# Kernel tuning notes

Hardware: AMD Instinct MI355X
Metric: run time of the kernel (lower is better)

The kernel has to match this reference:

```python
import jax, jax.numpy as jnp
import numpy as np

B, L, C = 4, 4096, 64

def setup_inputs() -> dict:
    key = jax.random.key(0)
    ks = jax.random.split(key, 7)
    s = 1.0 / np.sqrt(C)
    return {
        "x": jax.random.normal(ks[0], (B, L, C), dtype=jnp.float32),
        "Wq": jax.random.normal(ks[1], (C, C), dtype=jnp.float32) * s,
        "bq": jnp.zeros((C,), dtype=jnp.float32),
        "Wk": jax.random.normal(ks[2], (C, C), dtype=jnp.float32) * s,
        "bk": jnp.zeros((C,), dtype=jnp.float32),
        "Wv": jax.random.normal(ks[3], (C, C), dtype=jnp.float32) * s,
        "bv": jnp.zeros((C,), dtype=jnp.float32),
    }

def reference(x, Wq, bq, Wk, bk, Wv, bv):
    # Conv1D kernel_size=1 == pointwise linear over channels
    Q = jnp.einsum('blc,cf->blf', x, Wq) + bq  # [B, L, F]
    K = jnp.einsum('blc,cf->blf', x, Wk) + bk
    V = jnp.einsum('blc,cf->blf', x, Wv) + bv
    F = Wq.shape[1]
    scores = jnp.einsum('bqf,bkf->bqk', Q, K) / jnp.sqrt(jnp.float32(F))  # [B, Lq, Lk]
    # NOTE: original uses tf.keras.layers.Softmax(axis=1) -> normalize over QUERY axis
    attn = jax.nn.softmax(scores, axis=1)
    out = jnp.einsum('bqk,bkf->bqf', attn, V)
    return out + x
```

## Files before the change

kernel.cpp:

```cpp
#include <hip/hip_runtime.h>
#include <math.h>


#define BB 4
#define LL 4096
#define CC 64
#define C2 0.18033688011112042f

typedef __attribute__((ext_vector_type(8)))  short bf16x8;
typedef __attribute__((ext_vector_type(4)))  float f32x4;
typedef __attribute__((ext_vector_type(16))) float f32x16;
typedef __attribute__((ext_vector_type(4)))  unsigned int u32x4;

#define MFMA16(a, b, c) __builtin_amdgcn_mfma_f32_16x16x32_bf16(a, b, c, 0, 0, 0)
#define MFMA32(a, b, c) __builtin_amdgcn_mfma_f32_32x32x16_bf16(a, b, c, 0, 0, 0)
#define EXP2(x) __builtin_amdgcn_exp2f(x)

#define GLDS(gp, lp) __builtin_amdgcn_global_load_lds( \
    (const __attribute__((address_space(1))) unsigned int*)(gp), \
    (__attribute__((address_space(3))) unsigned int*)(lp), 16, 0, 0)
#define WAITVM0() asm volatile("s_waitcnt vmcnt(0)" ::: "memory")
#define WAITVM4() asm volatile("s_waitcnt vmcnt(4)" ::: "memory")
#define WAITVM8() asm volatile("s_waitcnt vmcnt(8)" ::: "memory")
#define LGKM0()   asm volatile("s_waitcnt lgkmcnt(0)" ::: "memory")
#define SBAR() __builtin_amdgcn_sched_barrier(0)

static __device__ __forceinline__ bf16x8 asbf(u32x4 v) {
    union { u32x4 a; bf16x8 b; } u; u.a = v; return u.b;
}
static __device__ __forceinline__ unsigned short f2bf(float f) {
    union { float f; unsigned u; } v; v.f = f;
    unsigned r = v.u + 0x7FFFu + ((v.u >> 16) & 1u);
    return (unsigned short)(r >> 16);
}
static __device__ __forceinline__ float bf2f(unsigned short h) {
    union { unsigned u; float f; } v; v.u = ((unsigned)h) << 16; return v.f;
}
static __device__ __forceinline__ bf16x8 pack8(float4 a, float4 b) {
    bf16x8 r;
    r[0] = (short)f2bf(a.x); r[1] = (short)f2bf(a.y);
    r[2] = (short)f2bf(a.z); r[3] = (short)f2bf(a.w);
    r[4] = (short)f2bf(b.x); r[5] = (short)f2bf(b.y);
    r[6] = (short)f2bf(b.z); r[7] = (short)f2bf(b.w);
    return r;
}
static __device__ __forceinline__ unsigned cvtpk(float lo, float hi) {
    unsigned r;
    asm("v_cvt_pk_bf16_f32 %0, %1, %2" : "=v"(r) : "v"(lo), "v"(hi));
    return r;
}


__global__ __launch_bounds__(512) void k_qkv(
    const float* __restrict__ x,
    const float* __restrict__ Wq, const float* __restrict__ bq,
    const float* __restrict__ Wk, const float* __restrict__ bk,
    const float* __restrict__ Wv, const float* __restrict__ bv,
    unsigned short* __restrict__ Qb, unsigned short* __restrict__ Kb,
    unsigned short* __restrict__ Vt)
{
    __shared__ float Wl[64 * 64];
    __shared__ unsigned short ldsV[64 * 72];
    __shared__ unsigned short ldsF[4096];
    const int bid = blockIdx.x;
    const int mat = bid % 3;
    const int r0 = (bid / 3) * 64;
    const int tid = threadIdx.x, w = tid >> 6, lane = tid & 63;
    const int c = lane & 15, g = lane >> 4;
    const int rw = (w >> 1) * 16;
    const int c0 = (w & 1) * 32;

    const float* W  = (mat == 0) ? Wq : (mat == 1) ? Wk : Wv;
    const float* bs = (mat == 0) ? bq : (mat == 1) ? bk : bv;

    {
        const float4* wsrc = (const float4*)W;
        float4* wdst = (float4*)Wl;
        wdst[tid] = wsrc[tid];
        wdst[tid + 512] = wsrc[tid + 512];
    }

    const float* xr = x + (size_t)(r0 + rw + c) * CC;
    const bf16x8 ax0 = pack8(((const float4*)xr)[2 * g], ((const float4*)xr)[2 * g + 1]);
    const bf16x8 ax1 = pack8(((const float4*)xr)[8 + 2 * g], ((const float4*)xr)[8 + 2 * g + 1]);
    __syncthreads();

    f32x4 acc0 = {0.f, 0.f, 0.f, 0.f}, acc1 = {0.f, 0.f, 0.f, 0.f};
    {
        const int col = c0 + c;
        bf16x8 b0, b1;
        #pragma unroll
        for (int j = 0; j < 8; ++j) {
            b0[j] = (short)f2bf(Wl[(8 * g + j) * 64 + col]);
            b1[j] = (short)f2bf(Wl[(32 + 8 * g + j) * 64 + col]);
        }
        acc0 = MFMA16(ax0, b0, acc0); acc0 = MFMA16(ax1, b1, acc0);
    }
    {
        const int col = c0 + 16 + c;
        bf16x8 b0, b1;
        #pragma unroll
        for (int j = 0; j < 8; ++j) {
            b0[j] = (short)f2bf(Wl[(8 * g + j) * 64 + col]);
            b1[j] = (short)f2bf(Wl[(32 + 8 * g + j) * 64 + col]);
        }
        acc1 = MFMA16(ax0, b0, acc1); acc1 = MFMA16(ax1, b1, acc1);
    }
    const float bias0 = bs[c0 + c], bias1 = bs[c0 + 16 + c];

    if (mat < 2) {
        #pragma unroll
        for (int r = 0; r < 4; ++r) {
            const int row = rw + 4 * g + r;
            const int tl = row >> 5, lr = row & 31;
            const int col0 = c0 + c;
            ldsF[tl * 2048 + (col0 >> 4) * 512 + (((col0 >> 3) & 1) * 32 + lr) * 8 + (col0 & 7)]
                = f2bf(acc0[r] + bias0);
            const int col1 = c0 + 16 + c;
            ldsF[tl * 2048 + (col1 >> 4) * 512 + (((col1 >> 3) & 1) * 32 + lr) * 8 + (col1 & 7)]
                = f2bf(acc1[r] + bias1);
        }
        __syncthreads();
        unsigned short* dst = (mat == 0) ? Qb : Kb;
        *(uint4*)(dst + ((size_t)(r0 >> 5)) * 2048 + tid * 8) =
            *(const uint4*)(ldsF + tid * 8);
    } else {
        #pragma unroll
        for (int r = 0; r < 4; ++r) {
            const int rowin = rw + 4 * g + r;
            ldsV[(c0 + c) * 72 + rowin]      = f2bf(acc0[r] + bias0);
            ldsV[(c0 + 16 + c) * 72 + rowin] = f2bf(acc1[r] + bias1);
        }
        __syncthreads();
        const int b = r0 >> 12, ktb = (r0 & 4095) >> 5;
        const int f = tid >> 3, ch = tid & 7;
        const size_t dtile = (size_t)(b * 128 + ktb + (ch >> 2));
        const size_t didx = dtile * 2048
            + (size_t)(((f >> 5) * 2 + ((ch >> 1) & 1)) * 512
                       + ((ch & 1) * 32 + (f & 31)) * 8);
        *(uint4*)(Vt + didx) = *(const uint4*)(ldsV + f * 72 + ch * 8);
    }
}

__global__ __launch_bounds__(512, 2) void k_stats(
    const unsigned short* __restrict__ Qb, const unsigned short* __restrict__ Kb,
    unsigned short* __restrict__ Vt)
{
    const int nb = ((blockIdx.x & 7) << 5) | (blockIdx.x >> 3);
    const int b = nb >> 6, kt = nb & 63;
    const int tid = threadIdx.x, w = tid >> 6, lane = tid & 63;
    const int l31 = lane & 31, hi = lane >> 5;
    const int w_u = __builtin_amdgcn_readfirstlane(w);

    __shared__ unsigned short qsm[8][2][2048];
    __shared__ float pl[8][64];
    __shared__ float rls[64];

    const char* Kt = (const char*)Kb + ((size_t)(b * 128 + kt * 2)) * 4096 + lane * 16;
    const bf16x8 akA0 = *(const bf16x8*)(Kt);
    const bf16x8 akA1 = *(const bf16x8*)(Kt + 1024);
    const bf16x8 akA2 = *(const bf16x8*)(Kt + 2048);
    const bf16x8 akA3 = *(const bf16x8*)(Kt + 3072);
    const bf16x8 akB0 = *(const bf16x8*)(Kt + 4096);
    const bf16x8 akB1 = *(const bf16x8*)(Kt + 5120);
    const bf16x8 akB2 = *(const bf16x8*)(Kt + 6144);
    const bf16x8 akB3 = *(const bf16x8*)(Kt + 7168);

    const char* const gQ = (const char*)Qb + ((size_t)(b * 128 + w * 16)) * 4096 + lane * 16;

    #define QISS(s_, buf_) do { \
        const char* _g = gQ + (size_t)(s_) * 4096; \
        char* _l = (char*)&qsm[w_u][buf_][0]; \
        GLDS(_g, _l);              GLDS(_g + 1024, _l + 1024); \
        GLDS(_g + 2048, _l + 2048); GLDS(_g + 3072, _l + 3072); \
    } while (0)

    QISS(0, 0); QISS(1, 1);

    f32x16 laccA = {}, laccB = {};
    #pragma unroll 2
    for (int s = 0; s < 16; ++s) {
        const int buf = s & 1;
        if (s < 15) { WAITVM4(); } else { WAITVM0(); }
        SBAR();
        const char* qp = (const char*)&qsm[w_u][buf][0] + lane * 16;
        const bf16x8 q0 = *(const bf16x8*)(qp);
        const bf16x8 q1 = *(const bf16x8*)(qp + 1024);
        const bf16x8 q2 = *(const bf16x8*)(qp + 2048);
        const bf16x8 q3 = *(const bf16x8*)(qp + 3072);
        LGKM0(); SBAR();
        if (s < 14) QISS(s + 2, buf);
        f32x16 TA = {}, TB = {};
        TA = MFMA32(akA0, q0, TA); TA = MFMA32(akA1, q1, TA);
        TA = MFMA32(akA2, q2, TA); TA = MFMA32(akA3, q3, TA);
        TB = MFMA32(akB0, q0, TB); TB = MFMA32(akB1, q1, TB);
        TB = MFMA32(akB2, q2, TB); TB = MFMA32(akB3, q3, TB);
        #pragma unroll
        for (int r = 0; r < 16; ++r) {
            laccA[r] += EXP2(TA[r] * C2);
            laccB[r] += EXP2(TB[r] * C2);
        }
    }
    #undef QISS

    #pragma unroll
    for (int r = 0; r < 16; ++r) {
        float va = laccA[r], vb = laccB[r];
        va += __shfl_xor(va, 1);  vb += __shfl_xor(vb, 1);
        va += __shfl_xor(va, 2);  vb += __shfl_xor(vb, 2);
        va += __shfl_xor(va, 4);  vb += __shfl_xor(vb, 4);
        va += __shfl_xor(va, 8);  vb += __shfl_xor(vb, 8);
        va += __shfl_xor(va, 16); vb += __shfl_xor(vb, 16);
        laccA[r] = va; laccB[r] = vb;
    }
    if (l31 == 0) {
        #pragma unroll
        for (int r = 0; r < 16; ++r) {
            const int kr = (r & 3) + 8 * (r >> 2) + 4 * hi;
            pl[w][kr]      = laccA[r];
            pl[w][32 + kr] = laccB[r];
        }
    }
    __syncthreads();
    if (tid < 64) {
        float L = 0.f;
        #pragma unroll
        for (int ww = 0; ww < 8; ++ww) L += pl[ww][tid];
        rls[tid] = 1.0f / L;
    }
    __syncthreads();

    #pragma unroll
    for (int i = 0; i < 2; ++i) {
        unsigned short* base = Vt + ((size_t)(b * 128 + kt * 2 + i)) * 2048;
        const int frag = tid >> 7, lane16 = (tid & 127) >> 1, j0 = (tid & 1) * 4;
        const int kin = (frag & 1) * 16 + (lane16 >> 5) * 8 + j0;
        ushort4 v = *(const ushort4*)(base + tid * 4);
        v.x = f2bf(bf2f(v.x) * rls[i * 32 + kin + 0]);
        v.y = f2bf(bf2f(v.y) * rls[i * 32 + kin + 1]);
        v.z = f2bf(bf2f(v.z) * rls[i * 32 + kin + 2]);
        v.w = f2bf(bf2f(v.w) * rls[i * 32 + kin + 3]);
        *(ushort4*)(base + tid * 4) = v;
    }
}

__global__ __launch_bounds__(512, 2) void k_out(
    const float* __restrict__ x,
    const unsigned short* __restrict__ Qb, const unsigned short* __restrict__ Kb,
    const unsigned short* __restrict__ Vt,
    float* __restrict__ out)
{
    const int nb = ((blockIdx.x & 7) << 5) | (blockIdx.x >> 3);
    const int b = nb >> 6, qt = nb & 63;
    const int q0 = qt * 64;
    const int tid = threadIdx.x, w = tid >> 6, lane = tid & 63;
    const int l31 = lane & 31, hi = lane >> 5;
    const int w_u = __builtin_amdgcn_readfirstlane(w);

    __shared__ unsigned short ksm[8][2][2048];
    __shared__ unsigned short vsm[8][2][2048];

    const char* Qt0 = (const char*)Qb + ((size_t)(b * 128 + qt * 2)) * 4096 + lane * 16;
    const bf16x8 qA0 = *(const bf16x8*)(Qt0);
    const bf16x8 qA1 = *(const bf16x8*)(Qt0 + 1024);
    const bf16x8 qA2 = *(const bf16x8*)(Qt0 + 2048);
    const bf16x8 qA3 = *(const bf16x8*)(Qt0 + 3072);
    const bf16x8 qB0 = *(const bf16x8*)(Qt0 + 4096);
    const bf16x8 qB1 = *(const bf16x8*)(Qt0 + 5120);
    const bf16x8 qB2 = *(const bf16x8*)(Qt0 + 6144);
    const bf16x8 qB3 = *(const bf16x8*)(Qt0 + 7168);

    const char* const gK = (const char*)Kb + ((size_t)(b * 128 + w * 16)) * 4096 + lane * 16;
    const char* const gV = (const char*)Vt + ((size_t)(b * 128 + w * 16)) * 4096 + lane * 16;

    #define ISS(s_, buf_) do { \
        const char* _gk = gK + (size_t)(s_) * 4096; \
        const char* _gv = gV + (size_t)(s_) * 4096; \
        char* _lk = (char*)&ksm[w_u][buf_][0]; \
        char* _lv = (char*)&vsm[w_u][buf_][0]; \
        GLDS(_gk, _lk);              GLDS(_gk + 1024, _lk + 1024); \
        GLDS(_gk + 2048, _lk + 2048); GLDS(_gk + 3072, _lk + 3072); \
        GLDS(_gv, _lv);              GLDS(_gv + 1024, _lv + 1024); \
        GLDS(_gv + 2048, _lv + 2048); GLDS(_gv + 3072, _lv + 3072); \
    } while (0)

    ISS(0, 0); ISS(1, 1);

    f32x16 oA0 = {}, oA1 = {}, oB0 = {}, oB1 = {};

    #pragma unroll 2
    for (int s = 0; s < 16; ++s) {
        const int buf = s & 1;
        if (s < 15) { WAITVM8(); } else { WAITVM0(); }
        SBAR();
        const char* kp = (const char*)&ksm[w_u][buf][0] + lane * 16;
        const char* vp = (const char*)&vsm[w_u][buf][0] + lane * 16;
        const bf16x8 a0  = *(const bf16x8*)(kp);
        const bf16x8 a1  = *(const bf16x8*)(kp + 1024);
        const bf16x8 a2  = *(const bf16x8*)(kp + 2048);
        const bf16x8 a3  = *(const bf16x8*)(kp + 3072);
        const bf16x8 v00 = *(const bf16x8*)(vp);
        const bf16x8 v01 = *(const bf16x8*)(vp + 1024);
        const bf16x8 v10 = *(const bf16x8*)(vp + 2048);
        const bf16x8 v11 = *(const bf16x8*)(vp + 3072);
        LGKM0(); SBAR();
        if (s < 14) ISS(s + 2, buf);
        f32x16 TA = {}, TB = {};
        TA = MFMA32(a0, qA0, TA); TA = MFMA32(a1, qA1, TA);
        TA = MFMA32(a2, qA2, TA); TA = MFMA32(a3, qA3, TA);
        TB = MFMA32(a0, qB0, TB); TB = MFMA32(a1, qB1, TB);
        TB = MFMA32(a2, qB2, TB); TB = MFMA32(a3, qB3, TB);
        unsigned a0u = cvtpk(EXP2(TA[0] * C2),  EXP2(TA[1] * C2));
        unsigned a1u = cvtpk(EXP2(TA[2] * C2),  EXP2(TA[3] * C2));
        unsigned a2u = cvtpk(EXP2(TA[4] * C2),  EXP2(TA[5] * C2));
        unsigned a3u = cvtpk(EXP2(TA[6] * C2),  EXP2(TA[7] * C2));
        unsigned a4u = cvtpk(EXP2(TA[8] * C2),  EXP2(TA[9] * C2));
        unsigned a5u = cvtpk(EXP2(TA[10] * C2), EXP2(TA[11] * C2));
        unsigned a6u = cvtpk(EXP2(TA[12] * C2), EXP2(TA[13] * C2));
        unsigned a7u = cvtpk(EXP2(TA[14] * C2), EXP2(TA[15] * C2));
        unsigned b0u = cvtpk(EXP2(TB[0] * C2),  EXP2(TB[1] * C2));
        unsigned b1u = cvtpk(EXP2(TB[2] * C2),  EXP2(TB[3] * C2));
        unsigned b2u = cvtpk(EXP2(TB[4] * C2),  EXP2(TB[5] * C2));
        unsigned b3u = cvtpk(EXP2(TB[6] * C2),  EXP2(TB[7] * C2));
        unsigned b4u = cvtpk(EXP2(TB[8] * C2),  EXP2(TB[9] * C2));
        unsigned b5u = cvtpk(EXP2(TB[10] * C2), EXP2(TB[11] * C2));
        unsigned b6u = cvtpk(EXP2(TB[12] * C2), EXP2(TB[13] * C2));
        unsigned b7u = cvtpk(EXP2(TB[14] * C2), EXP2(TB[15] * C2));
        asm volatile("s_nop 1");
        asm("v_permlane32_swap_b32 %0, %1" : "+v"(a0u), "+v"(a2u));
        asm("v_permlane32_swap_b32 %0, %1" : "+v"(a1u), "+v"(a3u));
        asm("v_permlane32_swap_b32 %0, %1" : "+v"(a4u), "+v"(a6u));
        asm("v_permlane32_swap_b32 %0, %1" : "+v"(a5u), "+v"(a7u));
        asm("v_permlane32_swap_b32 %0, %1" : "+v"(b0u), "+v"(b2u));
        asm("v_permlane32_swap_b32 %0, %1" : "+v"(b1u), "+v"(b3u));
        asm("v_permlane32_swap_b32 %0, %1" : "+v"(b4u), "+v"(b6u));
        asm("v_permlane32_swap_b32 %0, %1" : "+v"(b5u), "+v"(b7u));
        u32x4 fA1, fA2, fB1, fB2;
        fA1[0] = a0u; fA1[1] = a1u; fA1[2] = a2u; fA1[3] = a3u;
        fA2[0] = a4u; fA2[1] = a5u; fA2[2] = a6u; fA2[3] = a7u;
        fB1[0] = b0u; fB1[1] = b1u; fB1[2] = b2u; fB1[3] = b3u;
        fB2[0] = b4u; fB2[1] = b5u; fB2[2] = b6u; fB2[3] = b7u;
        oA0 = MFMA32(v00, asbf(fA1), oA0);
        oA0 = MFMA32(v01, asbf(fA2), oA0);
        oA1 = MFMA32(v10, asbf(fA1), oA1);
        oA1 = MFMA32(v11, asbf(fA2), oA1);
        oB0 = MFMA32(v00, asbf(fB1), oB0);
        oB0 = MFMA32(v01, asbf(fB2), oB0);
        oB1 = MFMA32(v10, asbf(fB1), oB1);
        oB1 = MFMA32(v11, asbf(fB2), oB1);
    }
    #undef ISS

    __syncthreads();
    float* ocomb = (float*)&ksm[0][0][0];
    for (int i = tid; i < 64 * 68; i += 512) ocomb[i] = 0.f;
    __syncthreads();
    #pragma unroll
    for (int r = 0; r < 16; ++r) {
        const int fr = (r & 3) + 8 * (r >> 2) + 4 * hi;
        atomicAdd(&ocomb[l31 * 68 + fr],             oA0[r]);
        atomicAdd(&ocomb[l31 * 68 + 32 + fr],        oA1[r]);
        atomicAdd(&ocomb[(32 + l31) * 68 + fr],      oB0[r]);
        atomicAdd(&ocomb[(32 + l31) * 68 + 32 + fr], oB1[r]);
    }
    __syncthreads();
    {
        const int q = tid >> 3, f8 = (tid & 7) * 8;
        const size_t row = (size_t)b * LL + q0 + q;
        const float4 xv0 = ((const float4*)(x + row * CC))[f8 >> 2];
        const float4 xv1 = ((const float4*)(x + row * CC))[(f8 >> 2) + 1];
        const float4 ov0 = *(const float4*)(&ocomb[q * 68 + f8]);
        const float4 ov1 = *(const float4*)(&ocomb[q * 68 + f8 + 4]);
        ((float4*)(out + row * CC))[f8 >> 2] =
            make_float4(xv0.x + ov0.x, xv0.y + ov0.y, xv0.z + ov0.z, xv0.w + ov0.w);
        ((float4*)(out + row * CC))[(f8 >> 2) + 1] =
            make_float4(xv1.x + ov1.x, xv1.y + ov1.y, xv1.z + ov1.z, xv1.w + ov1.w);
    }
}

extern "C" void kernel_launch(void* const* d_in, const int* in_sizes, int n_in,
                              void* d_out, int out_size, void* d_ws, size_t ws_size,
                              hipStream_t stream)
{
    const float* x  = (const float*)d_in[0];
    const float* Wq = (const float*)d_in[1];
    const float* bq = (const float*)d_in[2];
    const float* Wk = (const float*)d_in[3];
    const float* bk = (const float*)d_in[4];
    const float* Wv = (const float*)d_in[5];
    const float* bv = (const float*)d_in[6];
    float* out = (float*)d_out;

    const size_t n = (size_t)BB * LL * CC;
    unsigned short* Qb = (unsigned short*)d_ws;
    unsigned short* Kb = Qb + n;
    unsigned short* Vt = Kb + n;

    hipLaunchKernelGGL(k_qkv, dim3(3 * BB * LL / 64), dim3(512), 0, stream,
                       x, Wq, bq, Wk, bk, Wv, bv, Qb, Kb, Vt);
    hipLaunchKernelGGL(k_stats, dim3(BB * (LL / 64)), dim3(512), 0, stream,
                       Qb, Kb, Vt);
    hipLaunchKernelGGL(k_out, dim3(BB * (LL / 64)), dim3(512), 0, stream,
                       x, Qb, Kb, Vt, out);
}
```

Baseline: 91.66 us.

## Load K/V/Q tiles directly into registers instead of via LDS staging

Replaces the global_load_lds double-buffered LDS staging of Q (stats kernel) and K/V (output kernel) with direct global_load_dwordx4 into register double buffers. Loads are issued right after use and tracked with vmcnt waits, so the LDS round trip and lgkm waits go away. LDS use drops, and k_stats launch bounds rise to 3 blocks per SM for more occupancy. The cost is more VGPRs, and redundant wrap-around loads (index & 15) are issued at the loop tail and then drained.

Result: faster. 88.66 us (-3.3%).

```diff
diff --git a/kernel.cpp b/kernel.cpp
--- a/kernel.cpp
+++ b/kernel.cpp
@@ -16,13 +16,11 @@
 #define MFMA32(a, b, c) __builtin_amdgcn_mfma_f32_32x32x16_bf16(a, b, c, 0, 0, 0)
 #define EXP2(x) __builtin_amdgcn_exp2f(x)
 
-#define GLDS(gp, lp) __builtin_amdgcn_global_load_lds( \
-    (const __attribute__((address_space(1))) unsigned int*)(gp), \
-    (__attribute__((address_space(3))) unsigned int*)(lp), 16, 0, 0)
+#define GLD4(dst, voff, base, imm) \
+    asm volatile("global_load_dwordx4 %0, %1, %2 offset:%c3" \
+                 : "=v"(dst) : "v"(voff), "s"(base), "i"(imm))
+#define WAITVM(n) asm volatile("s_waitcnt vmcnt(" #n ")")
 #define WAITVM0() asm volatile("s_waitcnt vmcnt(0)" ::: "memory")
-#define WAITVM4() asm volatile("s_waitcnt vmcnt(4)" ::: "memory")
-#define WAITVM8() asm volatile("s_waitcnt vmcnt(8)" ::: "memory")
-#define LGKM0()   asm volatile("s_waitcnt lgkmcnt(0)" ::: "memory")
 #define SBAR() __builtin_amdgcn_sched_barrier(0)
 
 static __device__ __forceinline__ bf16x8 asbf(u32x4 v) {
@@ -49,7 +47,6 @@
     asm("v_cvt_pk_bf16_f32 %0, %1, %2" : "=v"(r) : "v"(lo), "v"(hi));
     return r;
 }
-
 
 __global__ __launch_bounds__(512) void k_qkv(
     const float* __restrict__ x,
@@ -142,7 +139,7 @@
     }
 }
 
-__global__ __launch_bounds__(512, 2) void k_stats(
+__global__ __launch_bounds__(512, 3) void k_stats(
     const unsigned short* __restrict__ Qb, const unsigned short* __restrict__ Kb,
     unsigned short* __restrict__ Vt)
 {
@@ -150,9 +147,7 @@
     const int b = nb >> 6, kt = nb & 63;
     const int tid = threadIdx.x, w = tid >> 6, lane = tid & 63;
     const int l31 = lane & 31, hi = lane >> 5;
-    const int w_u = __builtin_amdgcn_readfirstlane(w);
-
-    __shared__ unsigned short qsm[8][2][2048];
+
     __shared__ float pl[8][64];
     __shared__ float rls[64];
 
@@ -166,41 +161,43 @@
     const bf16x8 akB2 = *(const bf16x8*)(Kt + 6144);
     const bf16x8 akB3 = *(const bf16x8*)(Kt + 7168);
 
-    const char* const gQ = (const char*)Qb + ((size_t)(b * 128 + w * 16)) * 4096 + lane * 16;
-
-    #define QISS(s_, buf_) do { \
-        const char* _g = gQ + (size_t)(s_) * 4096; \
-        char* _l = (char*)&qsm[w_u][buf_][0]; \
-        GLDS(_g, _l);              GLDS(_g + 1024, _l + 1024); \
-        GLDS(_g + 2048, _l + 2048); GLDS(_g + 3072, _l + 3072); \
+    const char* const sQ = (const char*)Qb + (size_t)b * 128 * 4096;
+    const unsigned wqoff = (unsigned)(w * 16 * 4096 + lane * 16);
+
+    u32x4 qA0, qA1, qA2, qA3, qB0, qB1, qB2, qB3;
+    #define QISS(P, s_) do { \
+        const unsigned vo = wqoff + (unsigned)((s_) * 4096); \
+        GLD4(P##0, vo, sQ, 0);    GLD4(P##1, vo, sQ, 1024); \
+        GLD4(P##2, vo, sQ, 2048); GLD4(P##3, vo, sQ, 3072); \
     } while (0)
 
-    QISS(0, 0); QISS(1, 1);
+    QISS(qA, 0); QISS(qB, 1);
 
     f32x16 laccA = {}, laccB = {};
-    #pragma unroll 2
-    for (int s = 0; s < 16; ++s) {
-        const int buf = s & 1;
-        if (s < 15) { WAITVM4(); } else { WAITVM0(); }
-        SBAR();
-        const char* qp = (const char*)&qsm[w_u][buf][0] + lane * 16;
-        const bf16x8 q0 = *(const bf16x8*)(qp);
-        const bf16x8 q1 = *(const bf16x8*)(qp + 1024);
-        const bf16x8 q2 = *(const bf16x8*)(qp + 2048);
-        const bf16x8 q3 = *(const bf16x8*)(qp + 3072);
-        LGKM0(); SBAR();
-        if (s < 14) QISS(s + 2, buf);
-        f32x16 TA = {}, TB = {};
-        TA = MFMA32(akA0, q0, TA); TA = MFMA32(akA1, q1, TA);
-        TA = MFMA32(akA2, q2, TA); TA = MFMA32(akA3, q3, TA);
-        TB = MFMA32(akB0, q0, TB); TB = MFMA32(akB1, q1, TB);
-        TB = MFMA32(akB2, q2, TB); TB = MFMA32(akB3, q3, TB);
-        #pragma unroll
-        for (int r = 0; r < 16; ++r) {
-            laccA[r] += EXP2(TA[r] * C2);
-            laccB[r] += EXP2(TB[r] * C2);
-        }
-    }
+    #define QHALF(P, nsi) do { \
+        WAITVM(4); SBAR(); \
+        const bf16x8 q0 = asbf(P##0), q1 = asbf(P##1); \
+        const bf16x8 q2 = asbf(P##2), q3 = asbf(P##3); \
+        f32x16 TA = {}, TB = {}; \
+        TA = MFMA32(akA0, q0, TA); TA = MFMA32(akA1, q1, TA); \
+        TA = MFMA32(akA2, q2, TA); TA = MFMA32(akA3, q3, TA); \
+        TB = MFMA32(akB0, q0, TB); TB = MFMA32(akB1, q1, TB); \
+        TB = MFMA32(akB2, q2, TB); TB = MFMA32(akB3, q3, TB); \
+        SBAR(); \
+        QISS(P, (nsi) & 15); \
+        _Pragma("unroll") \
+        for (int r = 0; r < 16; ++r) { \
+            laccA[r] += EXP2(TA[r] * C2); \
+            laccB[r] += EXP2(TB[r] * C2); \
+        } \
+    } while (0)
+
+    for (int s = 0; s < 16; s += 2) {
+        QHALF(qA, s + 2);
+        QHALF(qB, s + 3);
+    }
+    WAITVM0();
+    #undef QHALF
     #undef QISS
 
     #pragma unroll
@@ -255,10 +252,8 @@
     const int q0 = qt * 64;
     const int tid = threadIdx.x, w = tid >> 6, lane = tid & 63;
     const int l31 = lane & 31, hi = lane >> 5;
-    const int w_u = __builtin_amdgcn_readfirstlane(w);
-
-    __shared__ unsigned short ksm[8][2][2048];
-    __shared__ unsigned short vsm[8][2][2048];
+
+    __shared__ float ocomb[64 * 68];
 
     const char* Qt0 = (const char*)Qb + ((size_t)(b * 128 + qt * 2)) * 4096 + lane * 16;
     const bf16x8 qA0 = *(const bf16x8*)(Qt0);
@@ -270,89 +265,95 @@
     const bf16x8 qB2 = *(const bf16x8*)(Qt0 + 6144);
     const bf16x8 qB3 = *(const bf16x8*)(Qt0 + 7168);
 
-    const char* const gK = (const char*)Kb + ((size_t)(b * 128 + w * 16)) * 4096 + lane * 16;
-    const char* const gV = (const char*)Vt + ((size_t)(b * 128 + w * 16)) * 4096 + lane * 16;
-
-    #define ISS(s_, buf_) do { \
-        const char* _gk = gK + (size_t)(s_) * 4096; \
-        const char* _gv = gV + (size_t)(s_) * 4096; \
-        char* _lk = (char*)&ksm[w_u][buf_][0]; \
-        char* _lv = (char*)&vsm[w_u][buf_][0]; \
-        GLDS(_gk, _lk);              GLDS(_gk + 1024, _lk + 1024); \
-        GLDS(_gk + 2048, _lk + 2048); GLDS(_gk + 3072, _lk + 3072); \
-        GLDS(_gv, _lv);              GLDS(_gv + 1024, _lv + 1024); \
-        GLDS(_gv + 2048, _lv + 2048); GLDS(_gv + 3072, _lv + 3072); \
+    const char* const sK = (const char*)Kb + (size_t)b * 128 * 4096;
+    const char* const sV = (const char*)Vt + (size_t)b * 128 * 4096;
+    const unsigned wOff = (unsigned)(w * 16 * 4096 + lane * 16);
+
+    u32x4 Ak0, Ak1, Ak2, Ak3, Av0, Av1, Av2, Av3;
+    u32x4 Bk0, Bk1, Bk2, Bk3, Bv0, Bv1, Bv2, Bv3;
+
+    #define KISS(P, s_) do { \
+        const unsigned vo = wOff + (unsigned)((s_) * 4096); \
+        GLD4(P##k0, vo, sK, 0);    GLD4(P##k1, vo, sK, 1024); \
+        GLD4(P##k2, vo, sK, 2048); GLD4(P##k3, vo, sK, 3072); \
     } while (0)
-
-    ISS(0, 0); ISS(1, 1);
+    #define VISS(P, s_) do { \
+        const unsigned vo = wOff + (unsigned)((s_) * 4096); \
+        GLD4(P##v0, vo, sV, 0);    GLD4(P##v1, vo, sV, 1024); \
+        GLD4(P##v2, vo, sV, 2048); GLD4(P##v3, vo, sV, 3072); \
+    } while (0)
+
+    KISS(A, 0); VISS(A, 0);
+    KISS(B, 1); VISS(B, 1);
 
     f32x16 oA0 = {}, oA1 = {}, oB0 = {}, oB1 = {};
 
-    #pragma unroll 2
-    for (int s = 0; s < 16; ++s) {
-        const int buf = s & 1;
-        if (s < 15) { WAITVM8(); } else { WAITVM0(); }
-        SBAR();
-        const char* kp = (const char*)&ksm[w_u][buf][0] + lane * 16;
-        const char* vp = (const char*)&vsm[w_u][buf][0] + lane * 16;
-        const bf16x8 a0  = *(const bf16x8*)(kp);
-        const bf16x8 a1  = *(const bf16x8*)(kp + 1024);
-        const bf16x8 a2  = *(const bf16x8*)(kp + 2048);
-        const bf16x8 a3  = *(const bf16x8*)(kp + 3072);
-        const bf16x8 v00 = *(const bf16x8*)(vp);
-        const bf16x8 v01 = *(const bf16x8*)(vp + 1024);
-        const bf16x8 v10 = *(const bf16x8*)(vp + 2048);
-        const bf16x8 v11 = *(const bf16x8*)(vp + 3072);
-        LGKM0(); SBAR();
-        if (s < 14) ISS(s + 2, buf);
-        f32x16 TA = {}, TB = {};
-        TA = MFMA32(a0, qA0, TA); TA = MFMA32(a1, qA1, TA);
-        TA = MFMA32(a2, qA2, TA); TA = MFMA32(a3, qA3, TA);
-        TB = MFMA32(a0, qB0, TB); TB = MFMA32(a1, qB1, TB);
-        TB = MFMA32(a2, qB2, TB); TB = MFMA32(a3, qB3, TB);
-        unsigned a0u = cvtpk(EXP2(TA[0] * C2),  EXP2(TA[1] * C2));
-        unsigned a1u = cvtpk(EXP2(TA[2] * C2),  EXP2(TA[3] * C2));
-        unsigned a2u = cvtpk(EXP2(TA[4] * C2),  EXP2(TA[5] * C2));
-        unsigned a3u = cvtpk(EXP2(TA[6] * C2),  EXP2(TA[7] * C2));
-        unsigned a4u = cvtpk(EXP2(TA[8] * C2),  EXP2(TA[9] * C2));
-        unsigned a5u = cvtpk(EXP2(TA[10] * C2), EXP2(TA[11] * C2));
-        unsigned a6u = cvtpk(EXP2(TA[12] * C2), EXP2(TA[13] * C2));
-        unsigned a7u = cvtpk(EXP2(TA[14] * C2), EXP2(TA[15] * C2));
-        unsigned b0u = cvtpk(EXP2(TB[0] * C2),  EXP2(TB[1] * C2));
-        unsigned b1u = cvtpk(EXP2(TB[2] * C2),  EXP2(TB[3] * C2));
-        unsigned b2u = cvtpk(EXP2(TB[4] * C2),  EXP2(TB[5] * C2));
-        unsigned b3u = cvtpk(EXP2(TB[6] * C2),  EXP2(TB[7] * C2));
-        unsigned b4u = cvtpk(EXP2(TB[8] * C2),  EXP2(TB[9] * C2));
-        unsigned b5u = cvtpk(EXP2(TB[10] * C2), EXP2(TB[11] * C2));
-        unsigned b6u = cvtpk(EXP2(TB[12] * C2), EXP2(TB[13] * C2));
-        unsigned b7u = cvtpk(EXP2(TB[14] * C2), EXP2(TB[15] * C2));
-        asm volatile("s_nop 1");
-        asm("v_permlane32_swap_b32 %0, %1" : "+v"(a0u), "+v"(a2u));
-        asm("v_permlane32_swap_b32 %0, %1" : "+v"(a1u), "+v"(a3u));
-        asm("v_permlane32_swap_b32 %0, %1" : "+v"(a4u), "+v"(a6u));
-        asm("v_permlane32_swap_b32 %0, %1" : "+v"(a5u), "+v"(a7u));
-        asm("v_permlane32_swap_b32 %0, %1" : "+v"(b0u), "+v"(b2u));
-        asm("v_permlane32_swap_b32 %0, %1" : "+v"(b1u), "+v"(b3u));
-        asm("v_permlane32_swap_b32 %0, %1" : "+v"(b4u), "+v"(b6u));
-        asm("v_permlane32_swap_b32 %0, %1" : "+v"(b5u), "+v"(b7u));
-        u32x4 fA1, fA2, fB1, fB2;
-        fA1[0] = a0u; fA1[1] = a1u; fA1[2] = a2u; fA1[3] = a3u;
-        fA2[0] = a4u; fA2[1] = a5u; fA2[2] = a6u; fA2[3] = a7u;
-        fB1[0] = b0u; fB1[1] = b1u; fB1[2] = b2u; fB1[3] = b3u;
-        fB2[0] = b4u; fB2[1] = b5u; fB2[2] = b6u; fB2[3] = b7u;
-        oA0 = MFMA32(v00, asbf(fA1), oA0);
-        oA0 = MFMA32(v01, asbf(fA2), oA0);
-        oA1 = MFMA32(v10, asbf(fA1), oA1);
-        oA1 = MFMA32(v11, asbf(fA2), oA1);
-        oB0 = MFMA32(v00, asbf(fB1), oB0);
-        oB0 = MFMA32(v01, asbf(fB2), oB0);
-        oB1 = MFMA32(v10, asbf(fB1), oB1);
-        oB1 = MFMA32(v11, asbf(fB2), oB1);
-    }
-    #undef ISS
-
-    __syncthreads();
-    float* ocomb = (float*)&ksm[0][0][0];
+    #define OHALF(P, nsi) do { \
+        WAITVM(12); SBAR(); \
+        const bf16x8 a0 = asbf(P##k0), a1 = asbf(P##k1); \
+        const bf16x8 a2 = asbf(P##k2), a3 = asbf(P##k3); \
+        f32x16 TA = {}, TB = {}; \
+        TA = MFMA32(a0, qA0, TA); TA = MFMA32(a1, qA1, TA); \
+        TA = MFMA32(a2, qA2, TA); TA = MFMA32(a3, qA3, TA); \
+        TB = MFMA32(a0, qB0, TB); TB = MFMA32(a1, qB1, TB); \
+        TB = MFMA32(a2, qB2, TB); TB = MFMA32(a3, qB3, TB); \
+        SBAR(); \
+        KISS(P, (nsi) & 15); \
+        unsigned u0 = cvtpk(EXP2(TA[0] * C2),  EXP2(TA[1] * C2)); \
+        unsigned u1 = cvtpk(EXP2(TA[2] * C2),  EXP2(TA[3] * C2)); \
+        unsigned u2 = cvtpk(EXP2(TA[4] * C2),  EXP2(TA[5] * C2)); \
+        unsigned u3 = cvtpk(EXP2(TA[6] * C2),  EXP2(TA[7] * C2)); \
+        unsigned u4 = cvtpk(EXP2(TA[8] * C2),  EXP2(TA[9] * C2)); \
+        unsigned u5 = cvtpk(EXP2(TA[10] * C2), EXP2(TA[11] * C2)); \
+        unsigned u6 = cvtpk(EXP2(TA[12] * C2), EXP2(TA[13] * C2)); \
+        unsigned u7 = cvtpk(EXP2(TA[14] * C2), EXP2(TA[15] * C2)); \
+        unsigned w0 = cvtpk(EXP2(TB[0] * C2),  EXP2(TB[1] * C2)); \
+        unsigned w1 = cvtpk(EXP2(TB[2] * C2),  EXP2(TB[3] * C2)); \
+        unsigned w2 = cvtpk(EXP2(TB[4] * C2),  EXP2(TB[5] * C2)); \
+        unsigned w3 = cvtpk(EXP2(TB[6] * C2),  EXP2(TB[7] * C2)); \
+        unsigned w4 = cvtpk(EXP2(TB[8] * C2),  EXP2(TB[9] * C2)); \
+        unsigned w5 = cvtpk(EXP2(TB[10] * C2), EXP2(TB[11] * C2)); \
+        unsigned w6 = cvtpk(EXP2(TB[12] * C2), EXP2(TB[13] * C2)); \
+        unsigned w7 = cvtpk(EXP2(TB[14] * C2), EXP2(TB[15] * C2)); \
+        asm volatile("s_nop 1"); \
+        asm("v_permlane32_swap_b32 %0, %1" : "+v"(u0), "+v"(u2)); \
+        asm("v_permlane32_swap_b32 %0, %1" : "+v"(u1), "+v"(u3)); \
+        asm("v_permlane32_swap_b32 %0, %1" : "+v"(u4), "+v"(u6)); \
+        asm("v_permlane32_swap_b32 %0, %1" : "+v"(u5), "+v"(u7)); \
+        asm("v_permlane32_swap_b32 %0, %1" : "+v"(w0), "+v"(w2)); \
+        asm("v_permlane32_swap_b32 %0, %1" : "+v"(w1), "+v"(w3)); \
+        asm("v_permlane32_swap_b32 %0, %1" : "+v"(w4), "+v"(w6)); \
+        asm("v_permlane32_swap_b32 %0, %1" : "+v"(w5), "+v"(w7)); \
+        u32x4 fA1, fA2, fB1, fB2; \
+        fA1[0] = u0; fA1[1] = u1; fA1[2] = u2; fA1[3] = u3; \
+        fA2[0] = u4; fA2[1] = u5; fA2[2] = u6; fA2[3] = u7; \
+        fB1[0] = w0; fB1[1] = w1; fB1[2] = w2; fB1[3] = w3; \
+        fB2[0] = w4; fB2[1] = w5; fB2[2] = w6; fB2[3] = w7; \
+        WAITVM(12); SBAR(); \
+        const bf16x8 v00 = asbf(P##v0), v01 = asbf(P##v1); \
+        const bf16x8 v10 = asbf(P##v2), v11 = asbf(P##v3); \
+        oA0 = MFMA32(v00, asbf(fA1), oA0); \
+        oA0 = MFMA32(v01, asbf(fA2), oA0); \
+        oA1 = MFMA32(v10, asbf(fA1), oA1); \
+        oA1 = MFMA32(v11, asbf(fA2), oA1); \
+        oB0 = MFMA32(v00, asbf(fB1), oB0); \
+        oB0 = MFMA32(v01, asbf(fB2), oB0); \
+        oB1 = MFMA32(v10, asbf(fB1), oB1); \
+        oB1 = MFMA32(v11, asbf(fB2), oB1); \
+        SBAR(); \
+        VISS(P, (nsi) & 15); \
+    } while (0)
+
+    for (int s = 0; s < 16; s += 2) {
+        OHALF(A, s + 2);
+        OHALF(B, s + 3);
+    }
+    WAITVM0();
+    #undef OHALF
+    #undef KISS
+    #undef VISS
+
+    __syncthreads();
     for (int i = tid; i < 64 * 68; i += 512) ocomb[i] = 0.f;
     __syncthreads();
     #pragma unroll
```
